# Performance work log

Hardware: AMD Instinct MI355X
Metric: run time of the kernel (lower is better)

The kernel has to match this reference:

```python
import jax, jax.numpy as jnp
import numpy as np

N, IN_DIM, H_DIM, POS_DIM, K, M, E, OUT_DIM = 50000, 256, 96, 32, 64, 128, 800000, 40
HID = H_DIM + POS_DIM  # 128

def _lin(key, fan_out, fan_in):
    k1, k2 = jax.random.split(key)
    bnd = 1.0 / np.sqrt(fan_in)
    W = jax.random.uniform(k1, (fan_out, fan_in), minval=-bnd, maxval=bnd, dtype=jnp.float32)
    b = jax.random.uniform(k2, (fan_out,), minval=-bnd, maxval=bnd, dtype=jnp.float32)
    return W, b

def setup_inputs() -> dict:
    key = jax.random.key(0)
    ks = jax.random.split(key, 12)
    x = jax.random.normal(ks[0], (N, IN_DIM), dtype=jnp.float32)
    eigenvectors = jax.random.normal(ks[1], (N, M), dtype=jnp.float32)
    eigenvalues = jax.random.uniform(ks[2], (M,), dtype=jnp.float32)
    edge_index = jax.random.randint(ks[3], (2, E), 0, N, dtype=jnp.int64)
    W_feat, b_feat = _lin(ks[4], H_DIM, IN_DIM)
    alpha = jax.random.uniform(ks[5], (K, POS_DIM), minval=-1/np.sqrt(K), maxval=1/np.sqrt(K), dtype=jnp.float32)
    Wl1, bl1 = _lin(ks[6], HID, HID)
    Wr1, _ = _lin(ks[7], HID, HID)
    Wl2, bl2 = _lin(ks[8], HID, HID)
    Wr2, _ = _lin(ks[9], HID, HID)
    W_ro, b_ro = _lin(ks[10], OUT_DIM, HID)
    return dict(x=x, eigenvectors=eigenvectors, eigenvalues=eigenvalues, edge_index=edge_index,
                W_feat=W_feat, b_feat=b_feat, alpha=alpha,
                Wl1=Wl1, bl1=bl1, Wr1=Wr1, Wl2=Wl2, bl2=bl2, Wr2=Wr2,
                W_ro=W_ro, b_ro=b_ro)

def _sage_conv(x, src, dst, Wl, bl, Wr):
    # PyG SAGEConv (mean aggr): out = lin_l(mean_{j->i} x_j) + lin_r(x_i)
    n = x.shape[0]
    agg = jax.ops.segment_sum(x[src], dst, num_segments=n)           # [N, HID]
    cnt = jax.ops.segment_sum(jnp.ones_like(dst, dtype=x.dtype), dst, num_segments=n)
    mean = agg / jnp.maximum(cnt, 1.0)[:, None]
    return mean @ Wl.T + bl + x @ Wr.T

def reference(x, eigenvectors, eigenvalues, edge_index,
              W_feat, b_feat, alpha, Wl1, bl1, Wr1, Wl2, bl2, Wr2, W_ro, b_ro):
    # normalize eigenvectors per column to [-1, 1]
    ev_min = jnp.min(eigenvectors, axis=0, keepdims=True)
    ev_max = jnp.max(eigenvectors, axis=0, keepdims=True)
    ev = (eigenvectors - ev_min) / (ev_max - ev_min) * 2.0 - 1.0
    # normalize eigenvalues to [-1, 1], Chebyshev basis via arccos/cos
    lmin, lmax = jnp.min(eigenvalues), jnp.max(eigenvalues)
    lam = (eigenvalues - lmin) / (lmax - lmin) * 2.0 - 1.0
    theta = jnp.arccos(lam)[:, None] * jnp.arange(K, dtype=lam.dtype)[None, :]  # [M, K]
    pe = jnp.cos(theta) @ alpha                                                  # [M, pos_dim]
    pos = ev @ pe                                                                # [N, pos_dim]
    h = jnp.concatenate([x @ W_feat.T + b_feat, pos], axis=-1)                   # [N, HID]
    src, dst = edge_index[0], edge_index[1]
    h = jax.nn.relu(_sage_conv(h, src, dst, Wl1, bl1, Wr1))
    h = jax.nn.relu(_sage_conv(h, src, dst, Wl2, bl2, Wr2))
    out = jax.nn.log_softmax(h @ W_ro.T + b_ro, axis=-1)
    return out, pe
```

## Files before the change

### kernel.cpp

```cpp
#include <hip/hip_runtime.h>
#include <math.h>

#define N        50000
#define IN_DIM   256
#define H_DIM    96
#define POS_DIM  32
#define KCH      64
#define M        128
#define NE       800000
#define OUT_DIM  40
#define HID      128
#define NSCAN    196
#define NTILES   ((N + 63) / 64)
#define NBK      391
#define BKCAP    2560
#define NSCATB   512
#define SREG     1563

typedef __attribute__((ext_vector_type(8))) short short8v;
typedef __attribute__((ext_vector_type(4))) float float4v;

__device__ __forceinline__ unsigned short f2bf(float f){
  unsigned u = __float_as_uint(f);
  u += 0x7fffu + ((u >> 16) & 1u);
  return (unsigned short)(u >> 16);
}
__device__ __forceinline__ float bf_lo(unsigned u){ return __uint_as_float(u << 16); }
__device__ __forceinline__ float bf_hi(unsigned u){ return __uint_as_float(u & 0xffff0000u); }

__device__ __forceinline__ unsigned enc_key(float f){
  unsigned u = __float_as_uint(f);
  return (u & 0x80000000u) ? ~u : (u | 0x80000000u);
}
__device__ __forceinline__ float dec_key(unsigned k){
  unsigned u = (k & 0x80000000u) ? (k ^ 0x80000000u) : ~k;
  return __uint_as_float(u);
}

__global__ void k_init(unsigned* __restrict__ encmn, unsigned* __restrict__ encmx,
                       short* __restrict__ WT_pos, float* __restrict__ bias_pos,
                       int* __restrict__ bkt_cnt){
  int i = blockIdx.x*blockDim.x + threadIdx.x;
  if (i < M){ encmn[i] = 0xFFFFFFFFu; encmx[i] = 0u; bias_pos[i] = 0.f; }
  if (i < M*M) WT_pos[i] = 0;
  if (i < NBK) bkt_cnt[i] = 0;
}

__global__ __launch_bounds__(256) void k_colminmax(const float* __restrict__ ev,
    unsigned* __restrict__ encmn, unsigned* __restrict__ encmx){
  __shared__ float4 smn[256], smx[256];
  int tid = threadIdx.x;
  int cg  = tid & 31;
  int rs  = blockIdx.x*8 + (tid >> 5);
  int stride = gridDim.x*8;
  float4 mn = make_float4( 3.4e38f,  3.4e38f,  3.4e38f,  3.4e38f);
  float4 mx = make_float4(-3.4e38f, -3.4e38f, -3.4e38f, -3.4e38f);
  #pragma unroll 4
  for (int r = rs; r < N; r += stride){
    float4 v = *(const float4*)&ev[(size_t)r*M + cg*4];
    mn.x = fminf(mn.x, v.x); mn.y = fminf(mn.y, v.y);
    mn.z = fminf(mn.z, v.z); mn.w = fminf(mn.w, v.w);
    mx.x = fmaxf(mx.x, v.x); mx.y = fmaxf(mx.y, v.y);
    mx.z = fmaxf(mx.z, v.z); mx.w = fmaxf(mx.w, v.w);
  }
  smn[tid] = mn; smx[tid] = mx;
  __syncthreads();
  for (int s = 128; s >= 32; s >>= 1){
    if (tid < s){
      float4 a = smn[tid], b = smn[tid + s];
      smn[tid] = make_float4(fminf(a.x,b.x), fminf(a.y,b.y), fminf(a.z,b.z), fminf(a.w,b.w));
      float4 c = smx[tid], d = smx[tid + s];
      smx[tid] = make_float4(fmaxf(c.x,d.x), fmaxf(c.y,d.y), fmaxf(c.z,d.z), fmaxf(c.w,d.w));
    }
    __syncthreads();
  }
  if (tid < 32){
    float4 a = smn[tid], b = smx[tid];
    atomicMin(&encmn[tid*4+0], enc_key(a.x));
    atomicMin(&encmn[tid*4+1], enc_key(a.y));
    atomicMin(&encmn[tid*4+2], enc_key(a.z));
    atomicMin(&encmn[tid*4+3], enc_key(a.w));
    atomicMax(&encmx[tid*4+0], enc_key(b.x));
    atomicMax(&encmx[tid*4+1], enc_key(b.y));
    atomicMax(&encmx[tid*4+2], enc_key(b.z));
    atomicMax(&encmx[tid*4+3], enc_key(b.w));
  }
}

__global__ __launch_bounds__(256) void k_pe(
    const float* __restrict__ eigval, const float* __restrict__ alpha,
    const unsigned* __restrict__ encmn, const unsigned* __restrict__ encmx,
    short* __restrict__ WT_pos, float* __restrict__ pe_raw,
    float* __restrict__ pe_out){
  __shared__ float rmn[128], rmx[128];
  int tid = threadIdx.x;
  if (tid < 128){ float v = eigval[tid]; rmn[tid] = v; rmx[tid] = v; }
  __syncthreads();
  for (int s = 64; s; s >>= 1){
    if (tid < s){ rmn[tid] = fminf(rmn[tid], rmn[tid+s]); rmx[tid] = fmaxf(rmx[tid], rmx[tid+s]); }
    __syncthreads();
  }
  float lmin = rmn[0], lmax = rmx[0];
  int g = blockIdx.x*256 + tid;
  int m = g >> 5, p = g & 31;
  float v = eigval[m];
  float lam = (v - lmin)/(lmax - lmin)*2.0f - 1.0f;
  lam = fminf(1.0f, fmaxf(-1.0f, lam));
  float t0 = 1.0f, t1 = lam;
  float acc = alpha[p] + lam*alpha[POS_DIM + p];
  float two_lam = lam + lam;
  #pragma unroll
  for (int k = 2; k < KCH; ++k){
    float t2 = fmaf(two_lam, t1, -t0);
    acc = fmaf(t2, alpha[k*POS_DIM + p], acc);
    t0 = t1; t1 = t2;
  }
  pe_out[g] = acc;
  pe_raw[g] = acc;
  float cmn = dec_key(encmn[m]);
  float cmx = dec_key(encmx[m]);
  float A = 2.0f/(cmx - cmn);
  WT_pos[p*M + m] = (short)f2bf(A*acc);
}

__global__ __launch_bounds__(256) void k_bias(
    const unsigned* __restrict__ encmn, const unsigned* __restrict__ encmx,
    const float* __restrict__ pe_raw, float* __restrict__ bias_pos){
  __shared__ float s[256];
  int tid = threadIdx.x;
  int p = tid >> 3, c = tid & 7;
  float sum = 0.f;
  for (int m = c*16; m < c*16 + 16; ++m){
    float cmn = dec_key(encmn[m]);
    float cmx = dec_key(encmx[m]);
    float A = 2.0f/(cmx - cmn);
    float B = -cmn*A - 1.0f;
    sum += B*pe_raw[m*POS_DIM + p];
  }
  s[tid] = sum;
  __syncthreads();
  if (c == 0){
    float t = 0.f;
    #pragma unroll
    for (int j = 0; j < 8; ++j) t += s[p*8 + j];
    bias_pos[p] = t;
  }
}

__global__ void k_prep_w(const float* __restrict__ Wf, const float* __restrict__ bfeat,
                         const float* __restrict__ Wl1, const float* __restrict__ Wr1,
                         const float* __restrict__ Wl2, const float* __restrict__ Wr2,
                         const float* __restrict__ Wro, const float* __restrict__ bro,
                         short* __restrict__ WTf, float* __restrict__ biasf,
                         short* __restrict__ Wc1, short* __restrict__ Wc2,
                         short* __restrict__ WTro, float* __restrict__ biasro){
  int i = blockIdx.x*256 + threadIdx.x;
  if (i < 128*256){
    int c = i >> 8, k = i & 255;
    WTf[i] = (c < H_DIM) ? (short)f2bf(Wf[c*IN_DIM + k]) : (short)0;
    Wc1[i] = (short)f2bf((k < HID) ? Wl1[c*HID + k] : Wr1[c*HID + k - HID]);
    Wc2[i] = (short)f2bf((k < HID) ? Wl2[c*HID + k] : Wr2[c*HID + k - HID]);
  }
  if (i < 48*128){
    int c = i >> 7, k = i & 127;
    WTro[i] = (c < OUT_DIM) ? (short)f2bf(Wro[c*HID + k]) : (short)0;
  }
  if (i < 128) biasf[i] = (i < H_DIM) ? bfeat[i] : 0.f;
  if (i >= 128 && i < 176) biasro[i - 128] = (i - 128 < OUT_DIM) ? bro[i - 128] : 0.f;
}

__global__ __launch_bounds__(256) void k_gemm_in(
    const float* __restrict__ x, const float* __restrict__ ev,
    const short* __restrict__ WTf, const float* __restrict__ biasf,
    const short* __restrict__ WT_pos, const float* __restrict__ bias_pos,
    unsigned short* __restrict__ outp)
{
  __shared__ short a_lds[64*384];
  int tid = threadIdx.x;
  int wid = tid >> 6, lane = tid & 63;
  int lrow = lane & 15, lk = (lane >> 4)*8;
  bool isPos = (wid == 3);

  short8v bfragF[8][2];
  short8v bfragP[4][2];
  float b0, b1;
  if (!isPos){
    int colBase = wid*32;
    #pragma unroll
    for (int s = 0; s < 8; ++s)
      #pragma unroll
      for (int ct = 0; ct < 2; ++ct){
        int col = colBase + ct*16 + lrow;
        bfragF[s][ct] = *(const short8v*)&WTf[col*256 + s*32 + lk];
      }
    b0 = biasf[colBase + lrow]; b1 = biasf[colBase + 16 + lrow];
  } else {
    #pragma unroll
    for (int s = 0; s < 4; ++s)
      #pragma unroll
      for (int ct = 0; ct < 2; ++ct){
        int col = ct*16 + lrow;
        bfragP[s][ct] = *(const short8v*)&WT_pos[col*128 + s*32 + lk];
      }
    b0 = bias_pos[lrow]; b1 = bias_pos[16 + lrow];
  }

  for (int tile = blockIdx.x; tile < NTILES; tile += gridDim.x){
    int n0 = tile*64;
    __syncthreads();
    for (int c = tid; c < 64*48; c += 256){
      int row = c / 48, k8 = c % 48;
      int gn = min(n0 + row, N-1);
      const float* src = (k8 < 32) ? &x[(size_t)gn*IN_DIM + k8*8]
                                   : &ev[(size_t)gn*M + (k8-32)*8];
      float4v f0 = *(const float4v*)src;
      float4v f1 = *(const float4v*)(src + 4);
      short8v vv;
      vv[0] = (short)f2bf(f0[0]); vv[1] = (short)f2bf(f0[1]);
      vv[2] = (short)f2bf(f0[2]); vv[3] = (short)f2bf(f0[3]);
      vv[4] = (short)f2bf(f1[0]); vv[5] = (short)f2bf(f1[1]);
      vv[6] = (short)f2bf(f1[2]); vv[7] = (short)f2bf(f1[3]);
      unsigned off = (unsigned)(row*768 + k8*16) ^ (unsigned)((row & 7) << 4);
      *(short8v*)((char*)a_lds + off) = vv;
    }
    __syncthreads();
    float4v acc[4][2];
    #pragma unroll
    for (int nt = 0; nt < 4; ++nt){
      acc[nt][0] = (float4v){0.f,0.f,0.f,0.f};
      acc[nt][1] = (float4v){0.f,0.f,0.f,0.f};
    }
    if (!isPos){
      #pragma unroll
      for (int s = 0; s < 8; ++s)
        #pragma unroll
        for (int nt = 0; nt < 4; ++nt){
          int row = nt*16 + lrow;
          unsigned off = (unsigned)(row*768 + (s*32 + lk)*2) ^ (unsigned)((row & 7) << 4);
          short8v a = *(const short8v*)((const char*)a_lds + off);
          acc[nt][0] = __builtin_amdgcn_mfma_f32_16x16x32_bf16(a, bfragF[s][0], acc[nt][0], 0, 0, 0);
          acc[nt][1] = __builtin_amdgcn_mfma_f32_16x16x32_bf16(a, bfragF[s][1], acc[nt][1], 0, 0, 0);
        }
    } else {
      #pragma unroll
      for (int s = 0; s < 4; ++s)
        #pragma unroll
        for (int nt = 0; nt < 4; ++nt){
          int row = nt*16 + lrow;
          unsigned off = (unsigned)(row*768 + 512 + (s*32 + lk)*2) ^ (unsigned)((row & 7) << 4);
          short8v a = *(const short8v*)((const char*)a_lds + off);
          acc[nt][0] = __builtin_amdgcn_mfma_f32_16x16x32_bf16(a, bfragP[s][0], acc[nt][0], 0, 0, 0);
          acc[nt][1] = __builtin_amdgcn_mfma_f32_16x16x32_bf16(a, bfragP[s][1], acc[nt][1], 0, 0, 0);
        }
    }
    int colBase = isPos ? 96 : wid*32;
    int rbase = (lane >> 4)*4;
    #pragma unroll
    for (int nt = 0; nt < 4; ++nt)
      #pragma unroll
      for (int ct = 0; ct < 2; ++ct){
        int col = colBase + ct*16 + lrow;
        float bb = ct ? b1 : b0;
        #pragma unroll
        for (int r = 0; r < 4; ++r){
          int node = n0 + nt*16 + rbase + r;
          if (node < N) outp[(size_t)node*HID + col] = f2bf(acc[nt][ct][r] + bb);
        }
      }
  }
}

__global__ __launch_bounds__(256) void k_conv(
    const short* __restrict__ A0, const short* __restrict__ A1,
    const short* __restrict__ WT, const float* __restrict__ bias,
    unsigned short* __restrict__ outp)
{
  __shared__ short a_lds[64*256];
  int tid = threadIdx.x;
  int wid = tid >> 6, lane = tid & 63;
  int colBase = wid*32;
  int lrow = lane & 15, lk = (lane >> 4)*8;

  short8v bfrag[8][2];
  #pragma unroll
  for (int s = 0; s < 8; ++s)
    #pragma unroll
    for (int ct = 0; ct < 2; ++ct){
      int col = colBase + ct*16 + lrow;
      bfrag[s][ct] = *(const short8v*)&WT[col*256 + s*32 + lk];
    }
  float b0 = bias[colBase + lrow], b1 = bias[colBase + 16 + lrow];

  for (int tile = blockIdx.x; tile < NTILES; tile += gridDim.x){
    int n0 = tile*64;
    __syncthreads();
    #pragma unroll
    for (int c = tid; c < 64*32; c += 256){
      int row = c >> 5, k8 = c & 31;
      int gn = min(n0 + row, N-1);
      const short* src = (k8 < 16) ? (A0 + (size_t)gn*HID + k8*8)
                                   : (A1 + (size_t)gn*HID + (k8-16)*8);
      short8v vv = *(const short8v*)src;
      unsigned off = (unsigned)(row*512 + k8*16) ^ (unsigned)((row & 7) << 4);
      *(short8v*)((char*)a_lds + off) = vv;
    }
    __syncthreads();
    float4v acc[4][2];
    #pragma unroll
    for (int nt = 0; nt < 4; ++nt){
      acc[nt][0] = (float4v){0.f,0.f,0.f,0.f};
      acc[nt][1] = (float4v){0.f,0.f,0.f,0.f};
    }
    #pragma unroll
    for (int s = 0; s < 8; ++s)
      #pragma unroll
      for (int nt = 0; nt < 4; ++nt){
        int row = nt*16 + lrow;
        unsigned off = (unsigned)(row*512 + (s*32 + lk)*2) ^ (unsigned)((row & 7) << 4);
        short8v a = *(const short8v*)((const char*)a_lds + off);
        acc[nt][0] = __builtin_amdgcn_mfma_f32_16x16x32_bf16(a, bfrag[s][0], acc[nt][0], 0, 0, 0);
        acc[nt][1] = __builtin_amdgcn_mfma_f32_16x16x32_bf16(a, bfrag[s][1], acc[nt][1], 0, 0, 0);
      }
    int rbase = (lane >> 4)*4;
    #pragma unroll
    for (int nt = 0; nt < 4; ++nt)
      #pragma unroll
      for (int ct = 0; ct < 2; ++ct){
        int col = colBase + ct*16 + lrow;
        float bb = ct ? b1 : b0;
        #pragma unroll
        for (int r = 0; r < 4; ++r){
          int node = n0 + nt*16 + rbase + r;
          if (node < N)
            outp[(size_t)node*HID + col] = f2bf(fmaxf(acc[nt][ct][r] + bb, 0.f));
        }
      }
  }
}

__global__ __launch_bounds__(256) void k_conv_ro(
    const short* __restrict__ A0, const short* __restrict__ A1,
    const short* __restrict__ WT, const float* __restrict__ bias,
    const short* __restrict__ WTro, const float* __restrict__ biasro,
    float* __restrict__ out)
{
  __shared__ short a_lds[64*256];
  __shared__ short o_lds[64*128];
  int tid = threadIdx.x;
  int wid = tid >> 6, lane = tid & 63;
  int colBase = wid*32;
  int lrow = lane & 15, lk = (lane >> 4)*8;

  short8v bfrag[8][2];
  #pragma unroll
  for (int s = 0; s < 8; ++s)
    #pragma unroll
    for (int ct = 0; ct < 2; ++ct){
      int col = colBase + ct*16 + lrow;
      bfrag[s][ct] = *(const short8v*)&WT[col*256 + s*32 + lk];
    }
  float b0 = bias[colBase + lrow], b1 = bias[colBase + 16 + lrow];

  short8v bfragR[4][3];
  #pragma unroll
  for (int s = 0; s < 4; ++s)
    #pragma unroll
    for (int t = 0; t < 3; ++t){
      int col = t*16 + lrow;
      bfragR[s][t] = *(const short8v*)&WTro[col*HID + s*32 + lk];
    }
  float biasR[3] = { biasro[lrow], biasro[16 + lrow], biasro[32 + lrow] };
  bool val2 = lrow < 8;

  for (int tile = blockIdx.x; tile < NTILES; tile += gridDim.x){
    int n0 = tile*64;
    __syncthreads();
    #pragma unroll
    for (int c = tid; c < 64*32; c += 256){
      int row = c >> 5, k8 = c & 31;
      int gn = min(n0 + row, N-1);
      const short* src = (k8 < 16) ? (A0 + (size_t)gn*HID + k8*8)
                                   : (A1 + (size_t)gn*HID + (k8-16)*8);
      short8v vv = *(const short8v*)src;
      unsigned off = (unsigned)(row*512 + k8*16) ^ (unsigned)((row & 7) << 4);
      *(short8v*)((char*)a_lds + off) = vv;
    }
    __syncthreads();
    float4v acc[4][2];
    #pragma unroll
    for (int nt = 0; nt < 4; ++nt){
      acc[nt][0] = (float4v){0.f,0.f,0.f,0.f};
      acc[nt][1] = (float4v){0.f,0.f,0.f,0.f};
    }
    #pragma unroll
    for (int s = 0; s < 8; ++s)
      #pragma unroll
      for (int nt = 0; nt < 4; ++nt){
        int row = nt*16 + lrow;
        unsigned off = (unsigned)(row*512 + (s*32 + lk)*2) ^ (unsigned)((row & 7) << 4);
        short8v a = *(const short8v*)((const char*)a_lds + off);
        acc[nt][0] = __builtin_amdgcn_mfma_f32_16x16x32_bf16(a, bfrag[s][0], acc[nt][0], 0, 0, 0);
        acc[nt][1] = __builtin_amdgcn_mfma_f32_16x16x32_bf16(a, bfrag[s][1], acc[nt][1], 0, 0, 0);
      }
    int rbase = (lane >> 4)*4;
    #pragma unroll
    for (int nt = 0; nt < 4; ++nt)
      #pragma unroll
      for (int ct = 0; ct < 2; ++ct){
        int col = colBase + ct*16 + lrow;
        float bb = ct ? b1 : b0;
        #pragma unroll
        for (int r = 0; r < 4; ++r){
          int row = nt*16 + rbase + r;
          float v = fmaxf(acc[nt][ct][r] + bb, 0.f);
          unsigned off = (unsigned)(row*256 + col*2) ^ (unsigned)((row & 7) << 4);
          *(short*)((char*)o_lds + off) = (short)f2bf(v);
        }
      }
    __syncthreads();
    float4v acc3[3];
    acc3[0] = (float4v){0.f,0.f,0.f,0.f};
    acc3[1] = (float4v){0.f,0.f,0.f,0.f};
    acc3[2] = (float4v){0.f,0.f,0.f,0.f};
    #pragma unroll
    for (int s = 0; s < 4; ++s){
      int row = wid*16 + lrow;
      unsigned off = (unsigned)(row*256 + (s*32 + lk)*2) ^ (unsigned)((row & 7) << 4);
      short8v a = *(const short8v*)((const char*)o_lds + off);
      acc3[0] = __builtin_amdgcn_mfma_f32_16x16x32_bf16(a, bfragR[s][0], acc3[0], 0, 0, 0);
      acc3[1] = __builtin_amdgcn_mfma_f32_16x16x32_bf16(a, bfragR[s][1], acc3[1], 0, 0, 0);
      acc3[2] = __builtin_amdgcn_mfma_f32_16x16x32_bf16(a, bfragR[s][2], acc3[2], 0, 0, 0);
    }
    #pragma unroll
    for (int r = 0; r < 4; ++r){
      float v0 = acc3[0][r] + biasR[0];
      float v1 = acc3[1][r] + biasR[1];
      float v2 = acc3[2][r] + biasR[2];
      float mx = fmaxf(v0, v1);
      mx = fmaxf(mx, val2 ? v2 : -3.4e38f);
      #pragma unroll
      for (int off = 1; off < 16; off <<= 1) mx = fmaxf(mx, __shfl_xor(mx, off, 64));
      float e = expf(v0 - mx) + expf(v1 - mx) + (val2 ? expf(v2 - mx) : 0.f);
      #pragma unroll
      for (int off = 1; off < 16; off <<= 1) e += __shfl_xor(e, off, 64);
      float lz = mx + logf(e);
      int node = n0 + wid*16 + (lane >> 4)*4 + r;
      if (node < N){
        out[(size_t)node*OUT_DIM + lrow]      = v0 - lz;
        out[(size_t)node*OUT_DIM + 16 + lrow] = v1 - lz;
        if (val2) out[(size_t)node*OUT_DIM + 32 + lrow] = v2 - lz;
      }
    }
  }
}

__global__ __launch_bounds__(256) void k_hist(const int* __restrict__ dst,
                                              int* __restrict__ bkt_cnt){
  __shared__ int h[NBK];
  int tid = threadIdx.x;
  for (int i = tid; i < NBK; i += 256) h[i] = 0;
  __syncthreads();
  for (int e = blockIdx.x*256 + tid; e < NE; e += gridDim.x*256)
    atomicAdd(&h[dst[e] >> 7], 1);
  __syncthreads();
  for (int i = tid; i < NBK; i += 256){
    int c = h[i];
    if (c) atomicAdd(&bkt_cnt[i], c);
  }
}

__global__ __launch_bounds__(512) void k_bktscan(const int* __restrict__ bkt_cnt,
    int* __restrict__ bkt_start, int* __restrict__ bkt_cursor){
  __shared__ int s[512];
  int t = threadIdx.x;
  int v = (t < NBK) ? bkt_cnt[t] : 0;
  s[t] = v;
  __syncthreads();
  for (int st = 1; st < 512; st <<= 1){
    int a = (t >= st) ? s[t-st] : 0;
    __syncthreads();
    s[t] += a;
    __syncthreads();
  }
  int excl = s[t] - v;
  if (t < NBK){ bkt_start[t] = excl; bkt_cursor[t] = excl; }
  if (t == 0) bkt_start[NBK] = NE;
}

__global__ __launch_bounds__(256) void k_bscatter(const int* __restrict__ src,
    const int* __restrict__ dst, int* __restrict__ bkt_cursor,
    unsigned* __restrict__ estage){
  __shared__ int lcnt[NBK];
  __shared__ int lbase[NBK];
  int tid = threadIdx.x;
  int e0 = blockIdx.x*SREG;
  int e1 = min(e0 + SREG, NE);
  for (int i = tid; i < NBK; i += 256) lcnt[i] = 0;
  __syncthreads();
  for (int e = e0 + tid; e < e1; e += 256)
    atomicAdd(&lcnt[dst[e] >> 7], 1);
  __syncthreads();
  for (int i = tid; i < NBK; i += 256){
    int c = lcnt[i];
    lbase[i] = c ? atomicAdd(&bkt_cursor[i], c) : 0;
    lcnt[i] = 0;
  }
  __syncthreads();
  for (int e = e0 + tid; e < e1; e += 256){
    int d = dst[e];
    int b = d >> 7;
    int slot = lbase[b] + atomicAdd(&lcnt[b], 1);
    estage[slot] = (unsigned)src[e] | ((unsigned)(d & 127) << 16);
  }
}

__global__ __launch_bounds__(256) void k_bcsr(const int* __restrict__ bkt_start,
    const unsigned* __restrict__ estage, unsigned short* __restrict__ csr,
    int* __restrict__ row_ptr){
  __shared__ unsigned eb[BKCAP];
  __shared__ int ncnt[128], sc[128], noff[128];
  int tid = threadIdx.x;
  int b = blockIdx.x;
  int s = bkt_start[b], e = bkt_start[b+1];
  int cnt = min(e - s, BKCAP);
  for (int i = tid; i < cnt; i += 256) eb[i] = estage[s + i];
  if (tid < 128) ncnt[tid] = 0;
  __syncthreads();
  for (int i = tid; i < cnt; i += 256)
    atomicAdd(&ncnt[(eb[i] >> 16) & 127], 1);
  __syncthreads();
  if (tid < 128) sc[tid] = ncnt[tid];
  __syncthreads();
  for (int st = 1; st < 128; st <<= 1){
    int a = (tid < 128 && tid >= st) ? sc[tid-st] : 0;
    __syncthreads();
    if (tid < 128) sc[tid] += a;
    __syncthreads();
  }
  if (tid < 128){
    int excl = sc[tid] - ncnt[tid];
    noff[tid] = excl;
    int node = b*128 + tid;
    if (node <= N) row_ptr[node] = s + excl;
    ncnt[tid] = 0;
  }
  __syncthreads();
  for (int i = tid; i < cnt; i += 256){
    unsigned v = eb[i];
    int ld = (v >> 16) & 127;
    int slot = noff[ld] + atomicAdd(&ncnt[ld], 1);
    csr[s + slot] = (unsigned short)(v & 0xffffu);
  }
}

__global__ __launch_bounds__(256) void k_agg_b(const unsigned* __restrict__ h,
    const int* __restrict__ row_ptr, const unsigned short* __restrict__ csr,
    unsigned* __restrict__ outm){
  int gid = blockIdx.x*blockDim.x + threadIdx.x;
  int i = gid >> 6;
  int lane = gid & 63;
  if (i >= N) return;
  int grp = lane >> 4;
  int lc  = lane & 15;
  int b = row_ptr[i], e = row_ptr[i+1];
  float a0[8] = {0.f,0.f,0.f,0.f,0.f,0.f,0.f,0.f};
  float a1[8] = {0.f,0.f,0.f,0.f,0.f,0.f,0.f,0.f};
  int j = b + grp;
  for (; j + 4 < e; j += 8){
    int s0 = csr[j];
    int s1 = csr[j+4];
    uint4 v0 = *(const uint4*)&h[(size_t)s0*64 + lc*4];
    uint4 v1 = *(const uint4*)&h[(size_t)s1*64 + lc*4];
    a0[0] += bf_lo(v0.x); a0[1] += bf_hi(v0.x);
    a0[2] += bf_lo(v0.y); a0[3] += bf_hi(v0.y);
    a0[4] += bf_lo(v0.z); a0[5] += bf_hi(v0.z);
    a0[6] += bf_lo(v0.w); a0[7] += bf_hi(v0.w);
    a1[0] += bf_lo(v1.x); a1[1] += bf_hi(v1.x);
    a1[2] += bf_lo(v1.y); a1[3] += bf_hi(v1.y);
    a1[4] += bf_lo(v1.z); a1[5] += bf_hi(v1.z);
    a1[6] += bf_lo(v1.w); a1[7] += bf_hi(v1.w);
  }
  if (j < e){
    int s0 = csr[j];
    uint4 v0 = *(const uint4*)&h[(size_t)s0*64 + lc*4];
    a0[0] += bf_lo(v0.x); a0[1] += bf_hi(v0.x);
    a0[2] += bf_lo(v0.y); a0[3] += bf_hi(v0.y);
    a0[4] += bf_lo(v0.z); a0[5] += bf_hi(v0.z);
    a0[6] += bf_lo(v0.w); a0[7] += bf_hi(v0.w);
  }
  #pragma unroll
  for (int k = 0; k < 8; ++k){
    float t = a0[k] + a1[k];
    t += __shfl_xor(t, 16, 64);
    t += __shfl_xor(t, 32, 64);
    a0[k] = t;
  }
  if (grp == 0){
    float inv = 1.0f / fmaxf((float)(e - b), 1.0f);
    uint4 o;
    o.x = (unsigned)f2bf(a0[0]*inv) | ((unsigned)f2bf(a0[1]*inv) << 16);
    o.y = (unsigned)f2bf(a0[2]*inv) | ((unsigned)f2bf(a0[3]*inv) << 16);
    o.z = (unsigned)f2bf(a0[4]*inv) | ((unsigned)f2bf(a0[5]*inv) << 16);
    o.w = (unsigned)f2bf(a0[6]*inv) | ((unsigned)f2bf(a0[7]*inv) << 16);
    *(uint4*)&outm[(size_t)i*64 + lc*4] = o;
  }
}

extern "C" void kernel_launch(void* const* d_in, const int* in_sizes, int n_in,
                              void* d_out, int out_size, void* d_ws, size_t ws_size,
                              hipStream_t stream){
  const float* x     = (const float*)d_in[0];
  const float* ev    = (const float*)d_in[1];
  const float* eigv  = (const float*)d_in[2];
  const int*   ei    = (const int*)d_in[3];
  const float* Wf    = (const float*)d_in[4];
  const float* bf    = (const float*)d_in[5];
  const float* alpha = (const float*)d_in[6];
  const float* Wl1   = (const float*)d_in[7];
  const float* bl1   = (const float*)d_in[8];
  const float* Wr1   = (const float*)d_in[9];
  const float* Wl2   = (const float*)d_in[10];
  const float* bl2   = (const float*)d_in[11];
  const float* Wr2   = (const float*)d_in[12];
  const float* Wro   = (const float*)d_in[13];
  const float* bro   = (const float*)d_in[14];
  float* out = (float*)d_out;

  short* h0b    = (short*)d_ws;
  short* h1b    = h0b + (size_t)N*HID;
  short* meanb  = h1b + (size_t)N*HID;
  short* WTf    = meanb + (size_t)N*HID;
  short* Wc1    = WTf + 128*256;
  short* Wc2    = Wc1 + 128*256;
  short* WT_pos = Wc2 + 128*256;
  short* WTro   = WT_pos + 128*128;
  float* biasf    = (float*)(WTro + 48*128);
  float* bias_pos = biasf + 128;
  float* biasro   = bias_pos + 128;
  unsigned* encmn = (unsigned*)(biasro + 48);
  unsigned* encmx = encmn + M;
  int* bkt_cnt    = (int*)(encmx + M);
  int* bkt_start  = bkt_cnt + NBK;
  int* bkt_cursor = bkt_start + NBK + 1;
  int* row_ptr    = bkt_cursor + NBK;
  unsigned* estage = (unsigned*)(row_ptr + N + 1);
  unsigned short* csr = (unsigned short*)(estage + NE);
  float* pe_raw = (float*)(csr + NE);

  const int* srcA = ei;
  const int* dstA = ei + NE;

  k_init<<<NSCAN, 256, 0, stream>>>(encmn, encmx, WT_pos, bias_pos, bkt_cnt);
  k_colminmax<<<256, 256, 0, stream>>>(ev, encmn, encmx);
  k_pe<<<16, 256, 0, stream>>>(eigv, alpha, encmn, encmx, WT_pos, pe_raw,
                               out + (size_t)N*OUT_DIM);
  k_bias<<<1, 256, 0, stream>>>(encmn, encmx, pe_raw, bias_pos);
  k_prep_w<<<128, 256, 0, stream>>>(Wf, bf, Wl1, Wr1, Wl2, Wr2, Wro, bro,
                                    WTf, biasf, Wc1, Wc2, WTro, biasro);
  k_hist<<<512, 256, 0, stream>>>(dstA, bkt_cnt);
  k_bktscan<<<1, 512, 0, stream>>>(bkt_cnt, bkt_start, bkt_cursor);
  k_bscatter<<<NSCATB, 256, 0, stream>>>(srcA, dstA, bkt_cursor, estage);
  k_bcsr<<<NBK, 256, 0, stream>>>(bkt_start, estage, csr, row_ptr);
  k_gemm_in<<<NTILES, 256, 0, stream>>>(x, ev, WTf, biasf, WT_pos, bias_pos,
                                        (unsigned short*)h0b);
  k_agg_b<<<(N*64)/256, 256, 0, stream>>>((const unsigned*)h0b, row_ptr, csr, (unsigned*)meanb);
  k_conv<<<NTILES, 256, 0, stream>>>(meanb, h0b, Wc1, bl1, (unsigned short*)h1b);
  k_agg_b<<<(N*64)/256, 256, 0, stream>>>((const unsigned*)h1b, row_ptr, csr, (unsigned*)meanb);
  k_conv_ro<<<NTILES, 256, 0, stream>>>(meanb, h1b, Wc2, bl2, WTro, biasro, out);
}
```

Before: 225.4 us.

## Fuse neighbor mean aggregation into SAGE conv GEMM kernels and merge weight prep

The separate CSR mean-aggregation kernels are removed. Each conv tile now gathers its 64 nodes' neighbor means directly into LDS (one wavefront per 16 rows) before the MFMA GEMM, which avoids writing and re-reading the intermediate mean buffer and saves two launches. Weight conversion is folded into the k_pe kernel, removing another launch. In exchange, the conv kernels become latency-bound gather loops with only NTILES blocks, so the irregular loads may be poorly overlapped. The k_pe kernel also now does more serial work across its 16 blocks.

```diff
diff --git a/kernel.cpp b/kernel.cpp
--- a/kernel.cpp
+++ b/kernel.cpp
@@ -90,8 +90,14 @@
 __global__ __launch_bounds__(256) void k_pe(
     const float* __restrict__ eigval, const float* __restrict__ alpha,
     const unsigned* __restrict__ encmn, const unsigned* __restrict__ encmx,
-    short* __restrict__ WT_pos, float* __restrict__ pe_raw,
-    float* __restrict__ pe_out){
+    const float* __restrict__ Wf, const float* __restrict__ bfeat,
+    const float* __restrict__ Wl1, const float* __restrict__ Wr1,
+    const float* __restrict__ Wl2, const float* __restrict__ Wr2,
+    const float* __restrict__ Wro, const float* __restrict__ bro,
+    short* __restrict__ WT_pos, float* __restrict__ pe_raw, float* __restrict__ pe_out,
+    short* __restrict__ WTf, float* __restrict__ biasf,
+    short* __restrict__ Wc1, short* __restrict__ Wc2,
+    short* __restrict__ WTro, float* __restrict__ biasro){
   __shared__ float rmn[128], rmx[128];
   int tid = threadIdx.x;
   if (tid < 128){ float v = eigval[tid]; rmn[tid] = v; rmx[tid] = v; }
@@ -121,6 +127,18 @@
   float cmx = dec_key(encmx[m]);
   float A = 2.0f/(cmx - cmn);
   WT_pos[p*M + m] = (short)f2bf(A*acc);
+  for (int i = g; i < 128*256; i += 4096){
+    int c = i >> 8, k = i & 255;
+    WTf[i] = (c < H_DIM) ? (short)f2bf(Wf[c*IN_DIM + k]) : (short)0;
+    Wc1[i] = (short)f2bf((k < HID) ? Wl1[c*HID + k] : Wr1[c*HID + k - HID]);
+    Wc2[i] = (short)f2bf((k < HID) ? Wl2[c*HID + k] : Wr2[c*HID + k - HID]);
+  }
+  for (int i = g; i < 48*128; i += 4096){
+    int c = i >> 7, k = i & 127;
+    WTro[i] = (c < OUT_DIM) ? (short)f2bf(Wro[c*HID + k]) : (short)0;
+  }
+  if (g < 128) biasf[g] = (g < H_DIM) ? bfeat[g] : 0.f;
+  if (g >= 128 && g < 176) biasro[g - 128] = (g - 128 < OUT_DIM) ? bro[g - 128] : 0.f;
 }
 
 __global__ __launch_bounds__(256) void k_bias(
@@ -145,28 +163,6 @@
     for (int j = 0; j < 8; ++j) t += s[p*8 + j];
     bias_pos[p] = t;
   }
-}
-
-__global__ void k_prep_w(const float* __restrict__ Wf, const float* __restrict__ bfeat,
-                         const float* __restrict__ Wl1, const float* __restrict__ Wr1,
-                         const float* __restrict__ Wl2, const float* __restrict__ Wr2,
-                         const float* __restrict__ Wro, const float* __restrict__ bro,
-                         short* __restrict__ WTf, float* __restrict__ biasf,
-                         short* __restrict__ Wc1, short* __restrict__ Wc2,
-                         short* __restrict__ WTro, float* __restrict__ biasro){
-  int i = blockIdx.x*256 + threadIdx.x;
-  if (i < 128*256){
-    int c = i >> 8, k = i & 255;
-    WTf[i] = (c < H_DIM) ? (short)f2bf(Wf[c*IN_DIM + k]) : (short)0;
-    Wc1[i] = (short)f2bf((k < HID) ? Wl1[c*HID + k] : Wr1[c*HID + k - HID]);
-    Wc2[i] = (short)f2bf((k < HID) ? Wl2[c*HID + k] : Wr2[c*HID + k - HID]);
-  }
-  if (i < 48*128){
-    int c = i >> 7, k = i & 127;
-    WTro[i] = (c < OUT_DIM) ? (short)f2bf(Wro[c*HID + k]) : (short)0;
-  }
-  if (i < 128) biasf[i] = (i < H_DIM) ? bfeat[i] : 0.f;
-  if (i >= 128 && i < 176) biasro[i - 128] = (i - 128 < OUT_DIM) ? bro[i - 128] : 0.f;
 }
 
 __global__ __launch_bounds__(256) void k_gemm_in(
@@ -270,16 +266,67 @@
   }
 }
 
-__global__ __launch_bounds__(256) void k_conv(
-    const short* __restrict__ A0, const short* __restrict__ A1,
+__device__ __forceinline__ void gather_mean_row(
+    const unsigned* __restrict__ hu, const int* __restrict__ row_ptr,
+    const unsigned short* __restrict__ csr, int node, int row,
+    int grp, int lc, short* a_lds)
+{
+  int b = row_ptr[node], e = row_ptr[node+1];
+  float a0[8] = {0.f,0.f,0.f,0.f,0.f,0.f,0.f,0.f};
+  float a1[8] = {0.f,0.f,0.f,0.f,0.f,0.f,0.f,0.f};
+  int j = b + grp;
+  for (; j + 4 < e; j += 8){
+    int s0 = csr[j];
+    int s1 = csr[j+4];
+    uint4 v0 = *(const uint4*)&hu[(size_t)s0*64 + lc*4];
+    uint4 v1 = *(const uint4*)&hu[(size_t)s1*64 + lc*4];
+    a0[0] += bf_lo(v0.x); a0[1] += bf_hi(v0.x);
+    a0[2] += bf_lo(v0.y); a0[3] += bf_hi(v0.y);
+    a0[4] += bf_lo(v0.z); a0[5] += bf_hi(v0.z);
+    a0[6] += bf_lo(v0.w); a0[7] += bf_hi(v0.w);
+    a1[0] += bf_lo(v1.x); a1[1] += bf_hi(v1.x);
+    a1[2] += bf_lo(v1.y); a1[3] += bf_hi(v1.y);
+    a1[4] += bf_lo(v1.z); a1[5] += bf_hi(v1.z);
+    a1[6] += bf_lo(v1.w); a1[7] += bf_hi(v1.w);
+  }
+  if (j < e){
+    int s0 = csr[j];
+    uint4 v0 = *(const uint4*)&hu[(size_t)s0*64 + lc*4];
+    a0[0] += bf_lo(v0.x); a0[1] += bf_hi(v0.x);
+    a0[2] += bf_lo(v0.y); a0[3] += bf_hi(v0.y);
+    a0[4] += bf_lo(v0.z); a0[5] += bf_hi(v0.z);
+    a0[6] += bf_lo(v0.w); a0[7] += bf_hi(v0.w);
+  }
+  #pragma unroll
+  for (int k = 0; k < 8; ++k){
+    float t = a0[k] + a1[k];
+    t += __shfl_xor(t, 16, 64);
+    t += __shfl_xor(t, 32, 64);
+    a0[k] = t;
+  }
+  if (grp == 0){
+    float inv = 1.0f / fmaxf((float)(e - b), 1.0f);
+    short8v mv;
+    #pragma unroll
+    for (int k = 0; k < 8; ++k) mv[k] = (short)f2bf(a0[k]*inv);
+    unsigned off = (unsigned)(row*512 + lc*16) ^ (unsigned)((row & 7) << 4);
+    *(short8v*)((char*)a_lds + off) = mv;
+  }
+}
+
+__global__ __launch_bounds__(256) void k_agg_conv(
+    const short* __restrict__ hprev, const int* __restrict__ row_ptr,
+    const unsigned short* __restrict__ csr,
     const short* __restrict__ WT, const float* __restrict__ bias,
     unsigned short* __restrict__ outp)
 {
   __shared__ short a_lds[64*256];
+  const unsigned* hu = (const unsigned*)hprev;
   int tid = threadIdx.x;
   int wid = tid >> 6, lane = tid & 63;
   int colBase = wid*32;
   int lrow = lane & 15, lk = (lane >> 4)*8;
+  int grp = lane >> 4, lc = lane & 15;
 
   short8v bfrag[8][2];
   #pragma unroll
@@ -295,14 +342,17 @@
     int n0 = tile*64;
     __syncthreads();
     #pragma unroll
-    for (int c = tid; c < 64*32; c += 256){
-      int row = c >> 5, k8 = c & 31;
+    for (int c = tid; c < 64*16; c += 256){
+      int row = c >> 4, k8 = c & 15;
       int gn = min(n0 + row, N-1);
-      const short* src = (k8 < 16) ? (A0 + (size_t)gn*HID + k8*8)
-                                   : (A1 + (size_t)gn*HID + (k8-16)*8);
-      short8v vv = *(const short8v*)src;
-      unsigned off = (unsigned)(row*512 + k8*16) ^ (unsigned)((row & 7) << 4);
+      short8v vv = *(const short8v*)(hprev + (size_t)gn*HID + k8*8);
+      unsigned off = (unsigned)(row*512 + (16 + k8)*16) ^ (unsigned)((row & 7) << 4);
       *(short8v*)((char*)a_lds + off) = vv;
+    }
+    for (int r = 0; r < 16; ++r){
+      int row = wid*16 + r;
+      int node = min(n0 + row, N-1);
+      gather_mean_row(hu, row_ptr, csr, node, row, grp, lc, a_lds);
     }
     __syncthreads();
     float4v acc[4][2];
@@ -338,18 +388,21 @@
   }
 }
 
-__global__ __launch_bounds__(256) void k_conv_ro(
-    const short* __restrict__ A0, const short* __restrict__ A1,
+__global__ __launch_bounds__(256) void k_agg_conv_ro(
+    const short* __restrict__ hprev, const int* __restrict__ row_ptr,
+    const unsigned short* __restrict__ csr,
     const short* __restrict__ WT, const float* __restrict__ bias,
     const short* __restrict__ WTro, const float* __restrict__ biasro,
     float* __restrict__ out)
 {
   __shared__ short a_lds[64*256];
   __shared__ short o_lds[64*128];
+  const unsigned* hu = (const unsigned*)hprev;
   int tid = threadIdx.x;
   int wid = tid >> 6, lane = tid & 63;
   int colBase = wid*32;
   int lrow = lane & 15, lk = (lane >> 4)*8;
+  int grp = lane >> 4, lc = lane & 15;
 
   short8v bfrag[8][2];
   #pragma unroll
@@ -376,14 +429,17 @@
     int n0 = tile*64;
     __syncthreads();
     #pragma unroll
-    for (int c = tid; c < 64*32; c += 256){
-      int row = c >> 5, k8 = c & 31;
+    for (int c = tid; c < 64*16; c += 256){
+      int row = c >> 4, k8 = c & 15;
       int gn = min(n0 + row, N-1);
-      const short* src = (k8 < 16) ? (A0 + (size_t)gn*HID + k8*8)
-                                   : (A1 + (size_t)gn*HID + (k8-16)*8);
-      short8v vv = *(const short8v*)src;
-      unsigned off = (unsigned)(row*512 + k8*16) ^ (unsigned)((row & 7) << 4);
+      short8v vv = *(const short8v*)(hprev + (size_t)gn*HID + k8*8);
+      unsigned off = (unsigned)(row*512 + (16 + k8)*16) ^ (unsigned)((row & 7) << 4);
       *(short8v*)((char*)a_lds + off) = vv;
+    }
+    for (int r = 0; r < 16; ++r){
+      int row = wid*16 + r;
+      int node = min(n0 + row, N-1);
+      gather_mean_row(hu, row_ptr, csr, node, row, grp, lc, a_lds);
     }
     __syncthreads();
     float4v acc[4][2];
@@ -550,59 +606,6 @@
     int ld = (v >> 16) & 127;
     int slot = noff[ld] + atomicAdd(&ncnt[ld], 1);
     csr[s + slot] = (unsigned short)(v & 0xffffu);
-  }
-}
-
-__global__ __launch_bounds__(256) void k_agg_b(const unsigned* __restrict__ h,
-    const int* __restrict__ row_ptr, const unsigned short* __restrict__ csr,
-    unsigned* __restrict__ outm){
-  int gid = blockIdx.x*blockDim.x + threadIdx.x;
-  int i = gid >> 6;
-  int lane = gid & 63;
-  if (i >= N) return;
-  int grp = lane >> 4;
-  int lc  = lane & 15;
-  int b = row_ptr[i], e = row_ptr[i+1];
-  float a0[8] = {0.f,0.f,0.f,0.f,0.f,0.f,0.f,0.f};
-  float a1[8] = {0.f,0.f,0.f,0.f,0.f,0.f,0.f,0.f};
-  int j = b + grp;
-  for (; j + 4 < e; j += 8){
-    int s0 = csr[j];
-    int s1 = csr[j+4];
-    uint4 v0 = *(const uint4*)&h[(size_t)s0*64 + lc*4];
-    uint4 v1 = *(const uint4*)&h[(size_t)s1*64 + lc*4];
-    a0[0] += bf_lo(v0.x); a0[1] += bf_hi(v0.x);
-    a0[2] += bf_lo(v0.y); a0[3] += bf_hi(v0.y);
-    a0[4] += bf_lo(v0.z); a0[5] += bf_hi(v0.z);
-    a0[6] += bf_lo(v0.w); a0[7] += bf_hi(v0.w);
-    a1[0] += bf_lo(v1.x); a1[1] += bf_hi(v1.x);
-    a1[2] += bf_lo(v1.y); a1[3] += bf_hi(v1.y);
-    a1[4] += bf_lo(v1.z); a1[5] += bf_hi(v1.z);
-    a1[6] += bf_lo(v1.w); a1[7] += bf_hi(v1.w);
-  }
-  if (j < e){
-    int s0 = csr[j];
-    uint4 v0 = *(const uint4*)&h[(size_t)s0*64 + lc*4];
-    a0[0] += bf_lo(v0.x); a0[1] += bf_hi(v0.x);
-    a0[2] += bf_lo(v0.y); a0[3] += bf_hi(v0.y);
-    a0[4] += bf_lo(v0.z); a0[5] += bf_hi(v0.z);
-    a0[6] += bf_lo(v0.w); a0[7] += bf_hi(v0.w);
-  }
-  #pragma unroll
-  for (int k = 0; k < 8; ++k){
-    float t = a0[k] + a1[k];
-    t += __shfl_xor(t, 16, 64);
-    t += __shfl_xor(t, 32, 64);
-    a0[k] = t;
-  }
-  if (grp == 0){
-    float inv = 1.0f / fmaxf((float)(e - b), 1.0f);
-    uint4 o;
-    o.x = (unsigned)f2bf(a0[0]*inv) | ((unsigned)f2bf(a0[1]*inv) << 16);
-    o.y = (unsigned)f2bf(a0[2]*inv) | ((unsigned)f2bf(a0[3]*inv) << 16);
-    o.z = (unsigned)f2bf(a0[4]*inv) | ((unsigned)f2bf(a0[5]*inv) << 16);
-    o.w = (unsigned)f2bf(a0[6]*inv) | ((unsigned)f2bf(a0[7]*inv) << 16);
-    *(uint4*)&outm[(size_t)i*64 + lc*4] = o;
   }
 }
 
@@ -652,19 +655,19 @@
 
   k_init<<<NSCAN, 256, 0, stream>>>(encmn, encmx, WT_pos, bias_pos, bkt_cnt);
   k_colminmax<<<256, 256, 0, stream>>>(ev, encmn, encmx);
-  k_pe<<<16, 256, 0, stream>>>(eigv, alpha, encmn, encmx, WT_pos, pe_raw,
-                               out + (size_t)N*OUT_DIM);
+  k_pe<<<16, 256, 0, stream>>>(eigv, alpha, encmn, encmx,
+                               Wf, bf, Wl1, Wr1, Wl2, Wr2, Wro, bro,
+                               WT_pos, pe_raw, out + (size_t)N*OUT_DIM,
+                               WTf, biasf, Wc1, Wc2, WTro, biasro);
   k_bias<<<1, 256, 0, stream>>>(encmn, encmx, pe_raw, bias_pos);
-  k_prep_w<<<128, 256, 0, stream>>>(Wf, bf, Wl1, Wr1, Wl2, Wr2, Wro, bro,
-                                    WTf, biasf, Wc1, Wc2, WTro, biasro);
   k_hist<<<512, 256, 0, stream>>>(dstA, bkt_cnt);
   k_bktscan<<<1, 512, 0, stream>>>(bkt_cnt, bkt_start, bkt_cursor);
   k_bscatter<<<NSCATB, 256, 0, stream>>>(srcA, dstA, bkt_cursor, estage);
   k_bcsr<<<NBK, 256, 0, stream>>>(bkt_start, estage, csr, row_ptr);
   k_gemm_in<<<NTILES, 256, 0, stream>>>(x, ev, WTf, biasf, WT_pos, bias_pos,
                                         (unsigned short*)h0b);
-  k_agg_b<<<(N*64)/256, 256, 0, stream>>>((const unsigned*)h0b, row_ptr, csr, (unsigned*)meanb);
-  k_conv<<<NTILES, 256, 0, stream>>>(meanb, h0b, Wc1, bl1, (unsigned short*)h1b);
-  k_agg_b<<<(N*64)/256, 256, 0, stream>>>((const unsigned*)h1b, row_ptr, csr, (unsigned*)meanb);
-  k_conv_ro<<<NTILES, 256, 0, stream>>>(meanb, h1b, Wc2, bl2, WTro, biasro, out);
-}
+  k_agg_conv<<<NTILES, 256, 0, stream>>>(h0b, row_ptr, csr, Wc1, bl1,
+                                         (unsigned short*)h1b);
+  k_agg_conv_ro<<<NTILES, 256, 0, stream>>>(h1b, row_ptr, csr, Wc2, bl2,
+                                            WTro, biasro, out);
+}
```

After: 372.3 us. 1.65x slower.
